# Kernel tuning notes

Hardware: AMD Instinct MI355X
Metric: run time of the kernel (lower is better)

## Reference

```python
import jax, jax.numpy as jnp
import numpy as np

B, C1, C2, H, W = 3, 256, 256, 48, 48
CC = 128      # c = int(c2*e)
NB = 2        # n blocks
HEADS = 4     # max(1, 128//32)
HD = CC // HEADS
SCALE = HD ** -0.5
EPS = 1e-5


def setup_inputs():
    key = jax.random.key(0)
    ks = iter(jax.random.split(key, 64))
    def rn(shape, scale=1.0):
        return jax.random.normal(next(ks), shape, jnp.float32) * scale
    s1 = 1.0 / np.sqrt(C1)
    sc = 1.0 / np.sqrt(CC)
    s2c = 1.0 / np.sqrt(2 * CC)
    s4c = 1.0 / np.sqrt(4 * CC)
    inp = {
        'x': rn((B, C1, H, W)),
        'cv1_w': rn((2 * CC, C1), s1),
        'cv1_g': 1.0 + rn((2 * CC,), 0.1), 'cv1_b': rn((2 * CC,), 0.1),
        'cv1_m': rn((2 * CC,), 0.1), 'cv1_v': 1.0 + 0.5 * jax.random.uniform(next(ks), (2 * CC,)),
        'n1_g': 1.0 + rn((NB, CC), 0.1), 'n1_b': rn((NB, CC), 0.1),
        'qkv_w': rn((NB, 3 * CC, CC), sc), 'qkv_b': rn((NB, 3 * CC), 0.02),
        'proj_w': rn((NB, CC, CC), sc), 'proj_b': rn((NB, CC), 0.02),
        'n2_g': 1.0 + rn((NB, CC), 0.1), 'n2_b': rn((NB, CC), 0.1),
        'f1_w': rn((NB, 2 * CC, CC), sc), 'f1_b': rn((NB, 2 * CC), 0.02),
        'f2_w': rn((NB, CC, 2 * CC), s2c), 'f2_b': rn((NB, CC), 0.02),
        'cv2_w': rn((C2, 4 * CC), s4c),
        'cv2_g': 1.0 + rn((C2,), 0.1), 'cv2_b': rn((C2,), 0.1),
        'cv2_m': rn((C2,), 0.1), 'cv2_v': 1.0 + 0.5 * jax.random.uniform(next(ks), (C2,)),
    }
    return inp


def conv1x1(x, w, b=None):
    y = jnp.einsum('bchw,oc->bohw', x, w)
    if b is not None:
        y = y + b[:, None, None]
    return y


def conv_bn_silu(x, w, g, b, m, v):
    y = conv1x1(x, w)
    y = (y - m[:, None, None]) / jnp.sqrt(v + EPS)[:, None, None] * g[:, None, None] + b[:, None, None]
    return jax.nn.silu(y)


def groupnorm1(x, g, b):
    mu = x.mean(axis=(1, 2, 3), keepdims=True)
    var = x.var(axis=(1, 2, 3), keepdims=True)
    return (x - mu) / jnp.sqrt(var + EPS) * g[:, None, None] + b[:, None, None]


def attention(x, qw, qb, pw, pb):
    # Faithful to torch code incl. the unbind(0)-over-batch quirk (requires B==3).
    b, c, h, w = x.shape
    qkv = conv1x1(x, qw, qb)                                   # (3, 3C, H, W)
    qkv = qkv.reshape(b, 3, HEADS, HD, h * w)                  # (B=3, 3, heads, hd, HW)
    q, k, v = qkv[0], qkv[1], qkv[2]                           # each (3, heads, hd, HW)
    attn = jnp.einsum('ghdn,ghdm->ghnm', q, k) * SCALE         # q.T @ k -> (3, heads, HW, HW)
    attn = jax.nn.softmax(attn, axis=-1)
    out = jnp.einsum('ghdm,ghnm->ghdn', v, attn)               # v @ attn.T -> (3, heads, hd, HW)
    out = out.transpose(0, 2, 1, 3).reshape(b, c, h, w)        # transpose(1,2).reshape
    return conv1x1(out, pw, pb)


def forward(x, cv1_w, cv1_g, cv1_b, cv1_m, cv1_v, n1_g, n1_b, qkv_w, qkv_b,
            proj_w, proj_b, n2_g, n2_b, f1_w, f1_b, f2_w, f2_b,
            cv2_w, cv2_g, cv2_b, cv2_m, cv2_v):
    y = conv_bn_silu(x, cv1_w, cv1_g, cv1_b, cv1_m, cv1_v)     # (B, 2c, H, W)
    y1, y2 = y[:, :CC], y[:, CC:]
    outs = [y1, y2]
    cur = y2
    for i in range(NB):
        a = attention(groupnorm1(cur, n1_g[i], n1_b[i]), qkv_w[i], qkv_b[i], proj_w[i], proj_b[i])
        cur = cur + a
        h2 = groupnorm1(cur, n2_g[i], n2_b[i])
        f = jax.nn.gelu(conv1x1(h2, f1_w[i], f1_b[i]), approximate=False)
        cur = cur + conv1x1(f, f2_w[i], f2_b[i])
        outs.append(cur)
    cat = jnp.concatenate(outs, axis=1)                        # (B, 4c, H, W)
    return conv_bn_silu(cat, cv2_w, cv2_g, cv2_b, cv2_m, cv2_v)


def reference(x, cv1_w, cv1_g, cv1_b, cv1_m, cv1_v, n1_g, n1_b, qkv_w, qkv_b,
              proj_w, proj_b, n2_g, n2_b, f1_w, f1_b, f2_w, f2_b,
              cv2_w, cv2_g, cv2_b, cv2_m, cv2_v):
    return forward(x, cv1_w, cv1_g, cv1_b, cv1_m, cv1_v, n1_g, n1_b, qkv_w, qkv_b,
                   proj_w, proj_b, n2_g, n2_b, f1_w, f1_b, f2_w, f2_b,
                   cv2_w, cv2_g, cv2_b, cv2_m, cv2_v)
```

## Files before the change

kernel.cpp:

```cpp
#include <hip/hip_runtime.h>
#include <hip/hip_bf16.h>
#include <math.h>

#define HW 2304
#define EPSV 1e-5f
#define INV_N (1.f / 294912.f)
#define QS_LOG2E (0.17677669529663687f * 1.44269504088896340f)
#define NSPLIT 4

enum { E_CV1 = 0, E_QKV = 1, E_RES = 2, E_F1 = 3, E_CV2 = 4 };

typedef __attribute__((ext_vector_type(8))) short bf16x8;
typedef __attribute__((ext_vector_type(4))) float f32x4;

static __device__ __forceinline__ ushort b16(float f) {
    union { __hip_bfloat16 h; ushort u; } cv;
    cv.h = __float2bfloat16(f);
    return cv.u;
}
static __device__ __forceinline__ float bf(ushort u) {
    union { unsigned u; float f; } c; c.u = (unsigned)u << 16; return c.f;
}
static __device__ __forceinline__ void stat_acc(float* STAT, int slot, int b,
                                                float s, float sq) {
    #pragma unroll
    for (int off = 32; off; off >>= 1) { s += __shfl_xor(s, off); sq += __shfl_xor(sq, off); }
    if ((threadIdx.x & 63) == 0) {
        atomicAdd(&STAT[(slot * 3 + b) * 2], s);
        atomicAdd(&STAT[(slot * 3 + b) * 2 + 1], sq);
    }
}

__global__ __launch_bounds__(256) void prep(
    const float* __restrict__ cv1w, const float* __restrict__ projw,
    const float* __restrict__ f2w, const float* __restrict__ cv2w,
    const float* __restrict__ qw, const float* __restrict__ g1, const float* __restrict__ b1,
    const float* __restrict__ fw1, const float* __restrict__ g2, const float* __restrict__ b2,
    const float* __restrict__ X,
    ushort* __restrict__ WB, ushort* __restrict__ FW, float* __restrict__ CV,
    ushort* __restrict__ XT, float* __restrict__ STAT)
{
    __shared__ ushort tb[64][68];
    const int bid = blockIdx.x, t = threadIdx.x;
    if (bid < 288) {
        if (bid == 0 && t < 32) STAT[t] = 0.f;
        const int idx = (bid * 256 + t) * 4;
        const float* src;
        int off;
        if      (idx < 65536)  { src = cv1w; off = 0; }
        else if (idx < 98304)  { src = projw; off = 65536; }
        else if (idx < 163840) { src = f2w;  off = 98304; }
        else                   { src = cv2w; off = 163840; }
        float4 v = *(const float4*)&src[idx - off];
        ushort4 u;
        u.x = b16(v.x); u.y = b16(v.y); u.z = b16(v.z); u.w = b16(v.w);
        *(ushort4*)&WB[idx] = u;
    } else if (bid < 608) {
        const int r = (bid - 288) * 4 + (t >> 6);
        const int lane = t & 63;
        const int i = r / 640, rr = r % 640;
        const float* wrow; const float* ga; const float* bb; ushort* dst;
        int cvs, cvb;
        if (rr < 384) {
            wrow = qw + ((size_t)i * 384 + rr) * 128;
            ga = g1 + i * 128; bb = b1 + i * 128;
            dst = FW + (size_t)i * 49152 + rr * 128;
            cvs = i * 1280 + rr; cvb = i * 1280 + 384 + rr;
        } else {
            const int o = rr - 384;
            wrow = fw1 + ((size_t)i * 256 + o) * 128;
            ga = g2 + i * 128; bb = b2 + i * 128;
            dst = FW + 98304 + (size_t)i * 32768 + o * 128;
            cvs = i * 1280 + 768 + o; cvb = i * 1280 + 1024 + o;
        }
        const float w0 = wrow[lane], w1 = wrow[lane + 64];
        const float p0 = w0 * ga[lane], p1 = w1 * ga[lane + 64];
        dst[lane] = b16(p0); dst[lane + 64] = b16(p1);
        float sw = p0 + p1;
        float wb = w0 * bb[lane] + w1 * bb[lane + 64];
        #pragma unroll
        for (int off = 32; off; off >>= 1) { sw += __shfl_xor(sw, off); wb += __shfl_xor(wb, off); }
        if (lane == 0) { CV[cvs] = sw; CV[cvb] = wb; }
    } else {
        const int flat = bid - 608;
        const int bx = flat % 36, by = (flat / 36) % 4, bz = flat / 144;
        const int cb = by * 64, nb = bx * 64;
        #pragma unroll
        for (int k = 0; k < 4; k++) {
            const int row = k * 16 + (t >> 4), cq = t & 15;
            float4 v = *(const float4*)&X[(size_t)(bz * 256 + cb + row) * HW + nb + cq * 4];
            ushort4 u; u.x = b16(v.x); u.y = b16(v.y); u.z = b16(v.z); u.w = b16(v.w);
            *(ushort4*)&tb[row][cq * 4] = u;
        }
        __syncthreads();
        #pragma unroll
        for (int k = 0; k < 4; k++) {
            const int n = k * 16 + (t >> 4), cq = t & 15;
            ushort4 u;
            u.x = tb[cq * 4 + 0][n]; u.y = tb[cq * 4 + 1][n];
            u.z = tb[cq * 4 + 2][n]; u.w = tb[cq * 4 + 3][n];
            *(ushort4*)&XT[((size_t)bz * HW + nb + n) * 256 + cb + cq * 4] = u;
        }
    }
}

template <int EPI>
__global__ __launch_bounds__(256) void gemm_mfma(
    const ushort* __restrict__ W, const ushort* __restrict__ X,
    int K, int xld, int xoff,
    const float* __restrict__ q0, const float* __restrict__ q1,
    const float* __restrict__ q2, const float* __restrict__ q3,
    float* __restrict__ STAT, int slotUse, int slotAcc,
    const float* __restrict__ cvec,
    ushort* __restrict__ CT, int rcol, int ycol,
    float* __restrict__ Yf,
    ushort* __restrict__ U0, ushort* __restrict__ U1, ushort* __restrict__ U2)
{
    const int b = blockIdx.z;
    const int t = threadIdx.x;
    const int w = t >> 6, l = t & 63;
    const int ln = l & 15, lg = l >> 4;
    const int wo = (w & 1) * 64, wn = (w >> 1) * 64;
    const int ob = blockIdx.y * 128 + wo;
    const int nb = blockIdx.x * 128 + wn;

    const ushort* ap = W + (size_t)(ob + ln) * K + lg * 8;
    const ushort* bp = X + ((size_t)b * HW + nb + ln) * xld + xoff + lg * 8;

    bf16x8 a0[4], bb0[4], a1[4], bb1[4];
    #pragma unroll
    for (int i = 0; i < 4; i++) {
        a0[i]  = *(const bf16x8*)(ap + (size_t)i * 16 * K);
        bb0[i] = *(const bf16x8*)(bp + (size_t)i * 16 * xld);
    }
    f32x4 acc[4][4];
    #pragma unroll
    for (int i = 0; i < 4; i++)
        #pragma unroll
        for (int j = 0; j < 4; j++) acc[i][j] = (f32x4){0.f, 0.f, 0.f, 0.f};

    for (int c0 = 32; c0 <= K; c0 += 32) {
        if (c0 < K) {
            #pragma unroll
            for (int i = 0; i < 4; i++) {
                a1[i]  = *(const bf16x8*)(ap + (size_t)i * 16 * K + c0);
                bb1[i] = *(const bf16x8*)(bp + (size_t)i * 16 * xld + c0);
            }
        }
        #pragma unroll
        for (int i = 0; i < 4; i++)
            #pragma unroll
            for (int j = 0; j < 4; j++)
                acc[i][j] = __builtin_amdgcn_mfma_f32_16x16x32_bf16(a0[i], bb0[j], acc[i][j], 0, 0, 0);
        #pragma unroll
        for (int i = 0; i < 4; i++) { a0[i] = a1[i]; bb0[i] = bb1[i]; }
    }

    float mu = 0.f, rs = 0.f;
    if (EPI == E_QKV || EPI == E_F1) {
        const float s  = STAT[(slotUse * 3 + b) * 2];
        const float sq = STAT[(slotUse * 3 + b) * 2 + 1];
        mu = s * INV_N;
        rs = rsqrtf(sq * INV_N - mu * mu + EPSV);
    }
    float ls = 0.f, lsq = 0.f;

    #pragma unroll
    for (int i = 0; i < 4; i++) {
        const int obase = ob + i * 16 + lg * 4;
        if (EPI == E_CV1 || EPI == E_CV2) {
            float sc[4], sh[4];
            #pragma unroll
            for (int r = 0; r < 4; r++) {
                const int o = obase + r;
                const float irs = rsqrtf(q3[o] + EPSV);
                sc[r] = q0[o] * irs;
                sh[r] = q1[o] - q2[o] * sc[r];
            }
            #pragma unroll
            for (int j = 0; j < 4; j++) {
                const int n = nb + j * 16 + ln;
                ushort4 u;
                #pragma unroll
                for (int r = 0; r < 4; r++) {
                    float y = fmaf(acc[i][j][r], sc[r], sh[r]);
                    y = y / (1.f + __expf(-y));
                    if (EPI == E_CV2) {
                        Yf[(size_t)(b * 256 + obase + r) * HW + n] = y;
                    } else {
                        ls += y; lsq += y * y;
                        if (r == 0) u.x = b16(y); else if (r == 1) u.y = b16(y);
                        else if (r == 2) u.z = b16(y); else u.w = b16(y);
                    }
                }
                if (EPI == E_CV1)
                    *(ushort4*)&CT[((size_t)b * HW + n) * 512 + ycol + obase] = u;
            }
        } else if (EPI == E_QKV) {
            const int gh = obase >> 5;
            const int d0 = obase & 31;
            float C[4];
            #pragma unroll
            for (int r = 0; r < 4; r++) {
                const int o = obase + r;
                C[r] = q0[o] + cvec[384 + o] - rs * mu * cvec[o];
            }
            #pragma unroll
            for (int j = 0; j < 4; j++) {
                const int n = nb + j * 16 + ln;
                float y0 = fmaf(rs, acc[i][j][0], C[0]);
                float y1 = fmaf(rs, acc[i][j][1], C[1]);
                float y2 = fmaf(rs, acc[i][j][2], C[2]);
                float y3 = fmaf(rs, acc[i][j][3], C[3]);
                if (b == 0) {
                    ushort4 u;
                    u.x = b16(y0 * QS_LOG2E); u.y = b16(y1 * QS_LOG2E);
                    u.z = b16(y2 * QS_LOG2E); u.w = b16(y3 * QS_LOG2E);
                    *(ushort4*)&U0[((size_t)gh * HW + n) * 32 + d0] = u;
                } else if (b == 1) {
                    ushort4 u;
                    u.x = b16(y0); u.y = b16(y1); u.z = b16(y2); u.w = b16(y3);
                    *(ushort4*)&U1[((size_t)gh * HW + n) * 32 + d0] = u;
                } else {
                    U2[(size_t)(obase + 0) * HW + n] = b16(y0);
                    U2[(size_t)(obase + 1) * HW + n] = b16(y1);
                    U2[(size_t)(obase + 2) * HW + n] = b16(y2);
                    U2[(size_t)(obase + 3) * HW + n] = b16(y3);
                }
            }
        } else if (EPI == E_RES) {
            #pragma unroll
            for (int j = 0; j < 4; j++) {
                const int n = nb + j * 16 + ln;
                const size_t base = ((size_t)b * HW + n) * 512;
                ushort4 rv = *(const ushort4*)&CT[base + rcol + obase];
                float y0 = acc[i][j][0] + q0[obase + 0] + bf(rv.x);
                float y1 = acc[i][j][1] + q0[obase + 1] + bf(rv.y);
                float y2 = acc[i][j][2] + q0[obase + 2] + bf(rv.z);
                float y3 = acc[i][j][3] + q0[obase + 3] + bf(rv.w);
                ls += (y0 + y1) + (y2 + y3);
                lsq += y0 * y0 + y1 * y1 + y2 * y2 + y3 * y3;
                ushort4 u;
                u.x = b16(y0); u.y = b16(y1); u.z = b16(y2); u.w = b16(y3);
                *(ushort4*)&CT[base + ycol + obase] = u;
            }
        } else {
            float C[4];
            #pragma unroll
            for (int r = 0; r < 4; r++) {
                const int o = obase + r;
                C[r] = q0[o] + cvec[256 + o] - rs * mu * cvec[o];
            }
            #pragma unroll
            for (int j = 0; j < 4; j++) {
                const int n = nb + j * 16 + ln;
                ushort4 u;
                #pragma unroll
                for (int r = 0; r < 4; r++) {
                    float y = fmaf(rs, acc[i][j][r], C[r]);
                    y = 0.5f * y * (1.f + erff(y * 0.70710678f));
                    if (r == 0) u.x = b16(y); else if (r == 1) u.y = b16(y);
                    else if (r == 2) u.z = b16(y); else u.w = b16(y);
                }
                *(ushort4*)&U0[((size_t)b * HW + n) * 256 + obase] = u;
            }
        }
    }
    if (EPI == E_CV1 && slotAcc >= 0 && blockIdx.y == 1) stat_acc(STAT, slotAcc, b, ls, lsq);
    if (EPI == E_RES && slotAcc >= 0) stat_acc(STAT, slotAcc, b, ls, lsq);
}

__global__ __launch_bounds__(256) void attn_mfma(
    const ushort* __restrict__ QT,
    const ushort* __restrict__ KT,
    const ushort* __restrict__ VB,
    float* __restrict__ POa,
    float* __restrict__ POb,
    float* __restrict__ MS)
{
    __shared__ __align__(16) ushort Kl[2][2048];
    __shared__ __align__(16) ushort Vl[2][2048];
    __shared__ __align__(16) ushort plds[4][16][72];
    const int gh = blockIdx.y, g = gh >> 2, h = gh & 3;
    const int sp = blockIdx.z;
    const int t = threadIdx.x, w = t >> 6, l = t & 63;
    const int ln = l & 15, lg = l >> 4;
    const int n0 = (blockIdx.x * 4 + w) * 16;
    const int ms0 = sp * 576, mend = ms0 + 576;

    const ushort* ktg = KT + (size_t)gh * HW * 32;
    const ushort* vg  = VB + ((size_t)g * 128 + h * 32) * HW;

    const int krow = t >> 2, kcq = t & 3;
    const int vrow = t >> 3, vcq = t & 7;
    const int kw = krow * 32 + ((kcq ^ (krow & 3)) << 3);
    const int vw = vrow * 64 + ((vcq ^ (vrow & 7)) << 3);
    const int krd = ln * 32 + ((lg ^ (ln & 3)) << 3);
    const int vs  = ln & 7;
    const int vrd0 = ln * 64 + ((lg ^ vs) << 3);
    const int vrd1 = ln * 64 + (((lg + 4) ^ vs) << 3);
    const int vrd2 = (16 + ln) * 64 + ((lg ^ vs) << 3);
    const int vrd3 = (16 + ln) * 64 + (((lg + 4) ^ vs) << 3);

    const bf16x8 qf = *(const bf16x8*)(QT + ((size_t)gh * HW + n0 + ln) * 32 + lg * 8);

    f32x4 o0 = {0.f, 0.f, 0.f, 0.f}, o1 = {0.f, 0.f, 0.f, 0.f};
    float M = -3.0e38f, S = 0.f;

    {
        bf16x8 kr = *(const bf16x8*)(ktg + (size_t)(ms0 + krow) * 32 + kcq * 8);
        bf16x8 vr = *(const bf16x8*)(vg + (size_t)vrow * HW + ms0 + vcq * 8);
        *(bf16x8*)&Kl[0][kw] = kr;
        *(bf16x8*)&Vl[0][vw] = vr;
    }
    int cur = 0;

    for (int m0 = ms0; m0 < mend; m0 += 64) {
        __syncthreads();
        const bool more = (m0 + 64 < mend);
        bf16x8 kr, vr;
        if (more) {
            kr = *(const bf16x8*)(ktg + (size_t)(m0 + 64 + krow) * 32 + kcq * 8);
            vr = *(const bf16x8*)(vg + (size_t)vrow * HW + m0 + 64 + vcq * 8);
        }

        f32x4 st[4];
        const f32x4 zero = {0.f, 0.f, 0.f, 0.f};
        #pragma unroll
        for (int mc = 0; mc < 4; mc++) {
            const bf16x8 kf = *(const bf16x8*)&Kl[cur][mc * 512 + krd];
            st[mc] = __builtin_amdgcn_mfma_f32_16x16x32_bf16(kf, qf, zero, 0, 0, 0);
        }

        float mx = st[0][0];
        #pragma unroll
        for (int mc = 0; mc < 4; mc++)
            #pragma unroll
            for (int r = 0; r < 4; r++) mx = fmaxf(mx, st[mc][r]);
        mx = fmaxf(mx, __shfl_xor(mx, 16));
        mx = fmaxf(mx, __shfl_xor(mx, 32));
        if (!__all(mx <= M + 8.f)) {
            const float Mn = fmaxf(M, mx);
            const float corr = exp2f(M - Mn);
            S *= corr;
            #pragma unroll
            for (int r = 0; r < 4; r++) { o0[r] *= corr; o1[r] *= corr; }
            M = Mn;
        }
        float ps = 0.f;
        ushort4 pw[4];
        #pragma unroll
        for (int mc = 0; mc < 4; mc++) {
            float p0v = exp2f(st[mc][0] - M), p1v = exp2f(st[mc][1] - M);
            float p2v = exp2f(st[mc][2] - M), p3v = exp2f(st[mc][3] - M);
            ps += (p0v + p1v) + (p2v + p3v);
            pw[mc].x = b16(p0v); pw[mc].y = b16(p1v);
            pw[mc].z = b16(p2v); pw[mc].w = b16(p3v);
        }
        ps += __shfl_xor(ps, 16);
        ps += __shfl_xor(ps, 32);
        S += ps;

        #pragma unroll
        for (int mc = 0; mc < 4; mc++)
            *(ushort4*)&plds[w][ln][mc * 16 + lg * 4] = pw[mc];
        bf16x8 pf0 = *(const bf16x8*)&plds[w][ln][lg * 8];
        bf16x8 pf1 = *(const bf16x8*)&plds[w][ln][32 + lg * 8];

        const bf16x8 vf0 = *(const bf16x8*)&Vl[cur][vrd0];
        const bf16x8 vf1 = *(const bf16x8*)&Vl[cur][vrd1];
        const bf16x8 vf2 = *(const bf16x8*)&Vl[cur][vrd2];
        const bf16x8 vf3 = *(const bf16x8*)&Vl[cur][vrd3];
        o0 = __builtin_amdgcn_mfma_f32_16x16x32_bf16(vf0, pf0, o0, 0, 0, 0);
        o0 = __builtin_amdgcn_mfma_f32_16x16x32_bf16(vf1, pf1, o0, 0, 0, 0);
        o1 = __builtin_amdgcn_mfma_f32_16x16x32_bf16(vf2, pf0, o1, 0, 0, 0);
        o1 = __builtin_amdgcn_mfma_f32_16x16x32_bf16(vf3, pf1, o1, 0, 0, 0);

        if (more) {
            *(bf16x8*)&Kl[cur ^ 1][kw] = kr;
            *(bf16x8*)&Vl[cur ^ 1][vw] = vr;
        }
        cur ^= 1;
    }

    float* po = (sp < 2) ? (POa + (size_t)sp * 884736)
                         : (POb + (size_t)(sp - 2) * 884736);
    #pragma unroll
    for (int r = 0; r < 4; r++) {
        const int d = lg * 4 + r;
        po[((size_t)gh * 32 + d) * HW + n0 + ln]      = o0[r];
        po[((size_t)gh * 32 + d + 16) * HW + n0 + ln] = o1[r];
    }
    if (lg == 0) {
        float* ms = MS + (((size_t)sp * 12 + gh) * HW + n0 + ln) * 2;
        ms[0] = M; ms[1] = S;
    }
}

__global__ __launch_bounds__(256) void merge_proj(
    const float* __restrict__ POa, const float* __restrict__ POb,
    const float* __restrict__ MS,
    const ushort* __restrict__ PW, const float* __restrict__ pb,
    ushort* __restrict__ CT, int rcol, int ycol,
    float* __restrict__ STAT, int slotAcc)
{
    __shared__ float fw[4][NSPLIT][64];
    __shared__ __align__(16) unsigned long long obuf[64][34];
    const int g = blockIdx.y, nb = blockIdx.x * 64;
    const int t = threadIdx.x;
    {
        const int h = t >> 6, nl = t & 63, gh = g * 4 + h, n = nb + nl;
        float Mk[NSPLIT], Sk[NSPLIT];
        #pragma unroll
        for (int k = 0; k < NSPLIT; k++) {
            Mk[k] = MS[(((size_t)k * 12 + gh) * HW + n) * 2 + 0];
            Sk[k] = MS[(((size_t)k * 12 + gh) * HW + n) * 2 + 1];
        }
        float Mx = Mk[0];
        #pragma unroll
        for (int k = 1; k < NSPLIT; k++) Mx = fmaxf(Mx, Mk[k]);
        float wk[NSPLIT], den = 0.f;
        #pragma unroll
        for (int k = 0; k < NSPLIT; k++) { wk[k] = exp2f(Mk[k] - Mx); den += Sk[k] * wk[k]; }
        const float inv = 1.f / den;
        #pragma unroll
        for (int k = 0; k < NSPLIT; k++) fw[h][k][nl] = wk[k] * inv;
    }
    __syncthreads();
    {
        const int nl = t & 63, dd = t >> 6;
        #pragma unroll
        for (int p = 0; p < 8; p++) {
            const int d = p * 4 + dd;
            ushort uu[4];
            #pragma unroll
            for (int h = 0; h < 4; h++) {
                const int gh = g * 4 + h;
                const size_t idx = ((size_t)gh * 32 + d) * HW + nb + nl;
                float v = 0.f;
                #pragma unroll
                for (int k = 0; k < 2; k++)
                    v += POa[(size_t)k * 884736 + idx] * fw[h][k][nl];
                #pragma unroll
                for (int k = 0; k < 2; k++)
                    v += POb[(size_t)k * 884736 + idx] * fw[h][k + 2][nl];
                uu[h] = b16(v);
            }
            obuf[nl][d] = (unsigned long long)uu[0] | ((unsigned long long)uu[1] << 16)
                        | ((unsigned long long)uu[2] << 32) | ((unsigned long long)uu[3] << 48);
        }
    }
    __syncthreads();
    const int w = t >> 6, l = t & 63, ln = l & 15, lg = l >> 4;
    const int wo = (w & 1) * 64, wn = (w >> 1) * 32;
    const ushort* ob_base = (const ushort*)&obuf[0][0];
    const ushort* ap = PW + (size_t)(wo + ln) * 128 + lg * 8;
    f32x4 acc[4][2];
    #pragma unroll
    for (int i = 0; i < 4; i++)
        #pragma unroll
        for (int jf = 0; jf < 2; jf++) acc[i][jf] = (f32x4){0.f, 0.f, 0.f, 0.f};
    #pragma unroll
    for (int kk = 0; kk < 4; kk++) {
        bf16x8 bfr[2];
        #pragma unroll
        for (int jf = 0; jf < 2; jf++)
            bfr[jf] = *(const bf16x8*)(ob_base + (wn + jf * 16 + ln) * 136 + kk * 32 + lg * 8);
        #pragma unroll
        for (int i = 0; i < 4; i++) {
            const bf16x8 af = *(const bf16x8*)(ap + (size_t)i * 16 * 128 + kk * 32);
            acc[i][0] = __builtin_amdgcn_mfma_f32_16x16x32_bf16(af, bfr[0], acc[i][0], 0, 0, 0);
            acc[i][1] = __builtin_amdgcn_mfma_f32_16x16x32_bf16(af, bfr[1], acc[i][1], 0, 0, 0);
        }
    }
    float ls = 0.f, lsq = 0.f;
    #pragma unroll
    for (int i = 0; i < 4; i++) {
        const int o4 = wo + i * 16 + lg * 4;
        #pragma unroll
        for (int jf = 0; jf < 2; jf++) {
            const int n = nb + wn + jf * 16 + ln;
            const size_t base = ((size_t)g * HW + n) * 512;
            ushort4 rv = *(const ushort4*)&CT[base + rcol + o4];
            float y0 = acc[i][jf][0] + pb[o4 + 0] + bf(rv.x);
            float y1 = acc[i][jf][1] + pb[o4 + 1] + bf(rv.y);
            float y2 = acc[i][jf][2] + pb[o4 + 2] + bf(rv.z);
            float y3 = acc[i][jf][3] + pb[o4 + 3] + bf(rv.w);
            ls += (y0 + y1) + (y2 + y3);
            lsq += y0 * y0 + y1 * y1 + y2 * y2 + y3 * y3;
            ushort4 u;
            u.x = b16(y0); u.y = b16(y1); u.z = b16(y2); u.w = b16(y3);
            *(ushort4*)&CT[base + ycol + o4] = u;
        }
    }
    stat_acc(STAT, slotAcc, g, ls, lsq);
}

extern "C" void kernel_launch(void* const* d_in, const int* in_sizes, int n_in,
                              void* d_out, int out_size, void* d_ws, size_t ws_size,
                              hipStream_t stream)
{
    (void)in_sizes; (void)n_in; (void)out_size; (void)ws_size;
    const float* x      = (const float*)d_in[0];
    const float* cv1_w  = (const float*)d_in[1];
    const float* cv1_g  = (const float*)d_in[2];
    const float* cv1_b  = (const float*)d_in[3];
    const float* cv1_m  = (const float*)d_in[4];
    const float* cv1_v  = (const float*)d_in[5];
    const float* n1_g   = (const float*)d_in[6];
    const float* n1_b   = (const float*)d_in[7];
    const float* qkv_w  = (const float*)d_in[8];
    const float* qkv_b  = (const float*)d_in[9];
    const float* proj_w = (const float*)d_in[10];
    const float* proj_b = (const float*)d_in[11];
    const float* n2_g   = (const float*)d_in[12];
    const float* n2_b   = (const float*)d_in[13];
    const float* f1_w   = (const float*)d_in[14];
    const float* f1_b   = (const float*)d_in[15];
    const float* f2_w   = (const float*)d_in[16];
    const float* f2_b   = (const float*)d_in[17];
    const float* cv2_w  = (const float*)d_in[18];
    const float* cv2_g  = (const float*)d_in[19];
    const float* cv2_b  = (const float*)d_in[20];
    const float* cv2_m  = (const float*)d_in[21];
    const float* cv2_v  = (const float*)d_in[22];
    float* out = (float*)d_out;

    float* ws = (float*)d_ws;
    ushort* CATT = (ushort*)ws;
    ushort* QT   = (ushort*)(ws + 1769472);
    ushort* KTb  = (ushort*)(ws + 2211840);
    ushort* VB   = (ushort*)(ws + 2654208);
    float*  MS   = ws + 3096576;
    ushort* WB   = (ushort*)(ws + 3428352);
    ushort* FW   = (ushort*)(ws + 3575808);
    float*  CV   = ws + 3657728;
    float*  STAT = ws + 3660288;
    float*  POb  = ws + 3660352;
    ushort* FT   = QT;
    ushort* XTX  = (ushort*)POb;
    float*  POa  = (float*)d_out;

    dim3 blk(256);

    prep<<<dim3(1040), blk, 0, stream>>>(
        cv1_w, proj_w, f2_w, cv2_w, qkv_w, n1_g, n1_b, f1_w, n2_g, n2_b,
        x, WB, FW, CV, XTX, STAT);

    gemm_mfma<E_CV1><<<dim3(18, 2, 3), blk, 0, stream>>>(
        WB + 0, XTX, 256, 256, 0, cv1_g, cv1_b, cv1_m, cv1_v,
        STAT, -1, 0, nullptr, CATT, 0, 0, nullptr, nullptr, nullptr, nullptr);

    for (int i = 0; i < 2; i++) {
        const int prev = (i == 0) ? 128 : 256;
        const int next = 256 + 128 * i;
        const int gn1 = (i == 0) ? 0 : 2;
        const int gn2 = (i == 0) ? 1 : 3;

        gemm_mfma<E_QKV><<<dim3(18, 3, 3), blk, 0, stream>>>(
            FW + (size_t)i * 49152, CATT, 128, 512, prev, qkv_b + i * 384,
            nullptr, nullptr, nullptr, STAT, gn1, -1, CV + i * 1280,
            nullptr, 0, 0, nullptr, QT, KTb, VB);
        attn_mfma<<<dim3(36, 12, NSPLIT), blk, 0, stream>>>(QT, KTb, VB, POa, POb, MS);
        merge_proj<<<dim3(36, 3), blk, 0, stream>>>(
            POa, POb, MS, WB + 65536 + (size_t)i * 16384, proj_b + i * 128,
            CATT, prev, next, STAT, gn2);

        gemm_mfma<E_F1><<<dim3(18, 2, 3), blk, 0, stream>>>(
            FW + 98304 + (size_t)i * 32768, CATT, 128, 512, next, f1_b + i * 256,
            nullptr, nullptr, nullptr, STAT, gn2, -1, CV + i * 1280 + 768,
            nullptr, 0, 0, nullptr, FT, nullptr, nullptr);
        gemm_mfma<E_RES><<<dim3(18, 1, 3), blk, 0, stream>>>(
            WB + 98304 + (size_t)i * 32768, FT, 256, 256, 0, f2_b + i * 128,
            nullptr, nullptr, nullptr, STAT, -1, (i == 0) ? 2 : -1, nullptr,
            CATT, next, next, nullptr, nullptr, nullptr, nullptr);
    }

    gemm_mfma<E_CV2><<<dim3(18, 2, 3), blk, 0, stream>>>(
        WB + 163840, CATT, 512, 512, 0, cv2_g, cv2_b, cv2_m, cv2_v,
        STAT, -1, -1, nullptr, nullptr, 0, 0, out, nullptr, nullptr, nullptr);
}
```

Baseline: 226.4 us.

## Fuse FFN f1/GELU/f2 GEMMs and final cv2 into one kernel per block

Replaces the separate F1 GEMM, F2 residual GEMM and final CV2 GEMM launches with a single ffn_fused kernel per block. Each 32-column tile computes the f1 output into LDS, runs f2 from LDS with the residual add, and in the last block also computes cv2 using the freshly written y tile from LDS. This removes the FT intermediate round trip through global memory and two to three kernel launches. In exchange the tiles are smaller (32 columns, 216 blocks), which lowers weight reuse and reloads the f1, f2 and cv2 weights from global memory for every tile.

```diff
diff --git a/kernel.cpp b/kernel.cpp
--- a/kernel.cpp
+++ b/kernel.cpp
@@ -8,7 +8,7 @@
 #define QS_LOG2E (0.17677669529663687f * 1.44269504088896340f)
 #define NSPLIT 4
 
-enum { E_CV1 = 0, E_QKV = 1, E_RES = 2, E_F1 = 3, E_CV2 = 4 };
+enum { E_CV1 = 0, E_QKV = 1 };
 
 typedef __attribute__((ext_vector_type(8))) short bf16x8;
 typedef __attribute__((ext_vector_type(4))) float f32x4;
@@ -112,8 +112,7 @@
     const float* __restrict__ q2, const float* __restrict__ q3,
     float* __restrict__ STAT, int slotUse, int slotAcc,
     const float* __restrict__ cvec,
-    ushort* __restrict__ CT, int rcol, int ycol,
-    float* __restrict__ Yf,
+    ushort* __restrict__ CT, int ycol,
     ushort* __restrict__ U0, ushort* __restrict__ U1, ushort* __restrict__ U2)
 {
     const int b = blockIdx.z;
@@ -157,7 +156,7 @@
     }
 
     float mu = 0.f, rs = 0.f;
-    if (EPI == E_QKV || EPI == E_F1) {
+    if (EPI == E_QKV) {
         const float s  = STAT[(slotUse * 3 + b) * 2];
         const float sq = STAT[(slotUse * 3 + b) * 2 + 1];
         mu = s * INV_N;
@@ -168,7 +167,7 @@
     #pragma unroll
     for (int i = 0; i < 4; i++) {
         const int obase = ob + i * 16 + lg * 4;
-        if (EPI == E_CV1 || EPI == E_CV2) {
+        if (EPI == E_CV1) {
             float sc[4], sh[4];
             #pragma unroll
             for (int r = 0; r < 4; r++) {
@@ -185,18 +184,13 @@
                 for (int r = 0; r < 4; r++) {
                     float y = fmaf(acc[i][j][r], sc[r], sh[r]);
                     y = y / (1.f + __expf(-y));
-                    if (EPI == E_CV2) {
-                        Yf[(size_t)(b * 256 + obase + r) * HW + n] = y;
-                    } else {
-                        ls += y; lsq += y * y;
-                        if (r == 0) u.x = b16(y); else if (r == 1) u.y = b16(y);
-                        else if (r == 2) u.z = b16(y); else u.w = b16(y);
-                    }
+                    ls += y; lsq += y * y;
+                    if (r == 0) u.x = b16(y); else if (r == 1) u.y = b16(y);
+                    else if (r == 2) u.z = b16(y); else u.w = b16(y);
                 }
-                if (EPI == E_CV1)
-                    *(ushort4*)&CT[((size_t)b * HW + n) * 512 + ycol + obase] = u;
-            }
-        } else if (EPI == E_QKV) {
+                *(ushort4*)&CT[((size_t)b * HW + n) * 512 + ycol + obase] = u;
+            }
+        } else {
             const int gh = obase >> 5;
             const int d0 = obase & 31;
             float C[4];
@@ -228,32 +222,67 @@
                     U2[(size_t)(obase + 3) * HW + n] = b16(y3);
                 }
             }
-        } else if (EPI == E_RES) {
-            #pragma unroll
-            for (int j = 0; j < 4; j++) {
-                const int n = nb + j * 16 + ln;
-                const size_t base = ((size_t)b * HW + n) * 512;
-                ushort4 rv = *(const ushort4*)&CT[base + rcol + obase];
-                float y0 = acc[i][j][0] + q0[obase + 0] + bf(rv.x);
-                float y1 = acc[i][j][1] + q0[obase + 1] + bf(rv.y);
-                float y2 = acc[i][j][2] + q0[obase + 2] + bf(rv.z);
-                float y3 = acc[i][j][3] + q0[obase + 3] + bf(rv.w);
-                ls += (y0 + y1) + (y2 + y3);
-                lsq += y0 * y0 + y1 * y1 + y2 * y2 + y3 * y3;
-                ushort4 u;
-                u.x = b16(y0); u.y = b16(y1); u.z = b16(y2); u.w = b16(y3);
-                *(ushort4*)&CT[base + ycol + obase] = u;
-            }
-        } else {
+        }
+    }
+    if (EPI == E_CV1 && slotAcc >= 0 && blockIdx.y == 1) stat_acc(STAT, slotAcc, b, ls, lsq);
+}
+
+template <int LAST>
+__global__ __launch_bounds__(256) void ffn_fused(
+    const ushort* __restrict__ FW1, const float* __restrict__ f1b,
+    const float* __restrict__ cvec,
+    const ushort* __restrict__ W2, const float* __restrict__ f2b,
+    ushort* __restrict__ CT, int col,
+    float* __restrict__ STAT, int slotUse, int slotAcc,
+    const ushort* __restrict__ WCV2, const float* __restrict__ q0,
+    const float* __restrict__ q1, const float* __restrict__ q2,
+    const float* __restrict__ q3, float* __restrict__ out)
+{
+    __shared__ __align__(16) ushort Fl[32][264];
+    __shared__ __align__(16) ushort Yl[32][136];
+    const int b = blockIdx.z, nb = blockIdx.x * 32;
+    const int t = threadIdx.x, w = t >> 6, l = t & 63;
+    const int ln = l & 15, lg = l >> 4;
+
+    const float s  = STAT[(slotUse * 3 + b) * 2];
+    const float sq = STAT[(slotUse * 3 + b) * 2 + 1];
+    const float mu = s * INV_N;
+    const float rs = rsqrtf(sq * INV_N - mu * mu + EPSV);
+
+    {
+        const int ob = w * 64;
+        const ushort* ap = FW1 + (size_t)(ob + ln) * 128 + lg * 8;
+        const ushort* bp = CT + ((size_t)b * HW + nb + ln) * 512 + col + lg * 8;
+        f32x4 acc[4][2];
+        #pragma unroll
+        for (int i = 0; i < 4; i++)
+            #pragma unroll
+            for (int j = 0; j < 2; j++) acc[i][j] = (f32x4){0.f, 0.f, 0.f, 0.f};
+        #pragma unroll
+        for (int kk = 0; kk < 4; kk++) {
+            bf16x8 bfr[2];
+            #pragma unroll
+            for (int j = 0; j < 2; j++)
+                bfr[j] = *(const bf16x8*)(bp + (size_t)(j * 16) * 512 + kk * 32);
+            #pragma unroll
+            for (int i = 0; i < 4; i++) {
+                const bf16x8 af = *(const bf16x8*)(ap + (size_t)(i * 16) * 128 + kk * 32);
+                acc[i][0] = __builtin_amdgcn_mfma_f32_16x16x32_bf16(af, bfr[0], acc[i][0], 0, 0, 0);
+                acc[i][1] = __builtin_amdgcn_mfma_f32_16x16x32_bf16(af, bfr[1], acc[i][1], 0, 0, 0);
+            }
+        }
+        #pragma unroll
+        for (int i = 0; i < 4; i++) {
+            const int obase = ob + i * 16 + lg * 4;
             float C[4];
             #pragma unroll
             for (int r = 0; r < 4; r++) {
                 const int o = obase + r;
-                C[r] = q0[o] + cvec[256 + o] - rs * mu * cvec[o];
-            }
-            #pragma unroll
-            for (int j = 0; j < 4; j++) {
-                const int n = nb + j * 16 + ln;
+                C[r] = f1b[o] + cvec[256 + o] - rs * mu * cvec[o];
+            }
+            #pragma unroll
+            for (int j = 0; j < 2; j++) {
+                const int n = j * 16 + ln;
                 ushort4 u;
                 #pragma unroll
                 for (int r = 0; r < 4; r++) {
@@ -262,12 +291,127 @@
                     if (r == 0) u.x = b16(y); else if (r == 1) u.y = b16(y);
                     else if (r == 2) u.z = b16(y); else u.w = b16(y);
                 }
-                *(ushort4*)&U0[((size_t)b * HW + n) * 256 + obase] = u;
-            }
-        }
-    }
-    if (EPI == E_CV1 && slotAcc >= 0 && blockIdx.y == 1) stat_acc(STAT, slotAcc, b, ls, lsq);
-    if (EPI == E_RES && slotAcc >= 0) stat_acc(STAT, slotAcc, b, ls, lsq);
+                *(ushort4*)&Fl[n][obase] = u;
+            }
+        }
+    }
+    __syncthreads();
+
+    float ls = 0.f, lsq = 0.f;
+    {
+        const int wo = w * 32;
+        const ushort* ap = W2 + (size_t)(wo + ln) * 256 + lg * 8;
+        f32x4 acc[2][2];
+        #pragma unroll
+        for (int i = 0; i < 2; i++)
+            #pragma unroll
+            for (int j = 0; j < 2; j++) acc[i][j] = (f32x4){0.f, 0.f, 0.f, 0.f};
+        #pragma unroll
+        for (int kk = 0; kk < 8; kk++) {
+            bf16x8 bfr[2];
+            #pragma unroll
+            for (int j = 0; j < 2; j++)
+                bfr[j] = *(const bf16x8*)&Fl[j * 16 + ln][kk * 32 + lg * 8];
+            #pragma unroll
+            for (int i = 0; i < 2; i++) {
+                const bf16x8 af = *(const bf16x8*)(ap + (size_t)(i * 16) * 256 + kk * 32);
+                acc[i][0] = __builtin_amdgcn_mfma_f32_16x16x32_bf16(af, bfr[0], acc[i][0], 0, 0, 0);
+                acc[i][1] = __builtin_amdgcn_mfma_f32_16x16x32_bf16(af, bfr[1], acc[i][1], 0, 0, 0);
+            }
+        }
+        #pragma unroll
+        for (int i = 0; i < 2; i++) {
+            const int o4 = wo + i * 16 + lg * 4;
+            #pragma unroll
+            for (int j = 0; j < 2; j++) {
+                const int n = nb + j * 16 + ln;
+                ushort* cp = &CT[((size_t)b * HW + n) * 512 + col + o4];
+                ushort4 rv = *(const ushort4*)cp;
+                float y0 = acc[i][j][0] + f2b[o4 + 0] + bf(rv.x);
+                float y1 = acc[i][j][1] + f2b[o4 + 1] + bf(rv.y);
+                float y2 = acc[i][j][2] + f2b[o4 + 2] + bf(rv.z);
+                float y3 = acc[i][j][3] + f2b[o4 + 3] + bf(rv.w);
+                ls += (y0 + y1) + (y2 + y3);
+                lsq += y0 * y0 + y1 * y1 + y2 * y2 + y3 * y3;
+                ushort4 u;
+                u.x = b16(y0); u.y = b16(y1); u.z = b16(y2); u.w = b16(y3);
+                *(ushort4*)cp = u;
+                if (LAST) *(ushort4*)&Yl[j * 16 + ln][o4] = u;
+            }
+        }
+    }
+    if (slotAcc >= 0) stat_acc(STAT, slotAcc, b, ls, lsq);
+
+    if (LAST) {
+        __syncthreads();
+        const int ob = w * 64;
+        const ushort* ap = WCV2 + (size_t)(ob + ln) * 512 + lg * 8;
+        const ushort* bp = CT + ((size_t)b * HW + nb + ln) * 512 + lg * 8;
+        f32x4 acc[4][2];
+        #pragma unroll
+        for (int i = 0; i < 4; i++)
+            #pragma unroll
+            for (int j = 0; j < 2; j++) acc[i][j] = (f32x4){0.f, 0.f, 0.f, 0.f};
+        bf16x8 a0[4], b0[2], a1[4], b1[2];
+        #pragma unroll
+        for (int i = 0; i < 4; i++) a0[i] = *(const bf16x8*)(ap + (size_t)(i * 16) * 512);
+        #pragma unroll
+        for (int j = 0; j < 2; j++) b0[j] = *(const bf16x8*)(bp + (size_t)(j * 16) * 512);
+        for (int c0 = 32; c0 <= 384; c0 += 32) {
+            if (c0 < 384) {
+                #pragma unroll
+                for (int i = 0; i < 4; i++)
+                    a1[i] = *(const bf16x8*)(ap + (size_t)(i * 16) * 512 + c0);
+                #pragma unroll
+                for (int j = 0; j < 2; j++)
+                    b1[j] = *(const bf16x8*)(bp + (size_t)(j * 16) * 512 + c0);
+            }
+            #pragma unroll
+            for (int i = 0; i < 4; i++) {
+                acc[i][0] = __builtin_amdgcn_mfma_f32_16x16x32_bf16(a0[i], b0[0], acc[i][0], 0, 0, 0);
+                acc[i][1] = __builtin_amdgcn_mfma_f32_16x16x32_bf16(a0[i], b0[1], acc[i][1], 0, 0, 0);
+            }
+            #pragma unroll
+            for (int i = 0; i < 4; i++) a0[i] = a1[i];
+            #pragma unroll
+            for (int j = 0; j < 2; j++) b0[j] = b1[j];
+        }
+        #pragma unroll
+        for (int kk = 0; kk < 4; kk++) {
+            bf16x8 bfr[2];
+            #pragma unroll
+            for (int j = 0; j < 2; j++)
+                bfr[j] = *(const bf16x8*)&Yl[j * 16 + ln][kk * 32 + lg * 8];
+            #pragma unroll
+            for (int i = 0; i < 4; i++) {
+                const bf16x8 af = *(const bf16x8*)(ap + (size_t)(i * 16) * 512 + 384 + kk * 32);
+                acc[i][0] = __builtin_amdgcn_mfma_f32_16x16x32_bf16(af, bfr[0], acc[i][0], 0, 0, 0);
+                acc[i][1] = __builtin_amdgcn_mfma_f32_16x16x32_bf16(af, bfr[1], acc[i][1], 0, 0, 0);
+            }
+        }
+        #pragma unroll
+        for (int i = 0; i < 4; i++) {
+            const int obase = ob + i * 16 + lg * 4;
+            float sc[4], sh[4];
+            #pragma unroll
+            for (int r = 0; r < 4; r++) {
+                const int o = obase + r;
+                const float irs = rsqrtf(q3[o] + EPSV);
+                sc[r] = q0[o] * irs;
+                sh[r] = q1[o] - q2[o] * sc[r];
+            }
+            #pragma unroll
+            for (int j = 0; j < 2; j++) {
+                const int n = nb + j * 16 + ln;
+                #pragma unroll
+                for (int r = 0; r < 4; r++) {
+                    float y = fmaf(acc[i][j][r], sc[r], sh[r]);
+                    y = y / (1.f + __expf(-y));
+                    out[(size_t)(b * 256 + obase + r) * HW + n] = y;
+                }
+            }
+        }
+    }
 }
 
 __global__ __launch_bounds__(256) void attn_mfma(
@@ -537,7 +681,6 @@
     float*  CV   = ws + 3657728;
     float*  STAT = ws + 3660288;
     float*  POb  = ws + 3660352;
-    ushort* FT   = QT;
     ushort* XTX  = (ushort*)POb;
     float*  POa  = (float*)d_out;
 
@@ -549,7 +692,7 @@
 
     gemm_mfma<E_CV1><<<dim3(18, 2, 3), blk, 0, stream>>>(
         WB + 0, XTX, 256, 256, 0, cv1_g, cv1_b, cv1_m, cv1_v,
-        STAT, -1, 0, nullptr, CATT, 0, 0, nullptr, nullptr, nullptr, nullptr);
+        STAT, -1, 0, nullptr, CATT, 0, nullptr, nullptr, nullptr);
 
     for (int i = 0; i < 2; i++) {
         const int prev = (i == 0) ? 128 : 256;
@@ -560,23 +703,22 @@
         gemm_mfma<E_QKV><<<dim3(18, 3, 3), blk, 0, stream>>>(
             FW + (size_t)i * 49152, CATT, 128, 512, prev, qkv_b + i * 384,
             nullptr, nullptr, nullptr, STAT, gn1, -1, CV + i * 1280,
-            nullptr, 0, 0, nullptr, QT, KTb, VB);
+            nullptr, 0, QT, KTb, VB);
         attn_mfma<<<dim3(36, 12, NSPLIT), blk, 0, stream>>>(QT, KTb, VB, POa, POb, MS);
         merge_proj<<<dim3(36, 3), blk, 0, stream>>>(
             POa, POb, MS, WB + 65536 + (size_t)i * 16384, proj_b + i * 128,
             CATT, prev, next, STAT, gn2);
 
-        gemm_mfma<E_F1><<<dim3(18, 2, 3), blk, 0, stream>>>(
-            FW + 98304 + (size_t)i * 32768, CATT, 128, 512, next, f1_b + i * 256,
-            nullptr, nullptr, nullptr, STAT, gn2, -1, CV + i * 1280 + 768,
-            nullptr, 0, 0, nullptr, FT, nullptr, nullptr);
-        gemm_mfma<E_RES><<<dim3(18, 1, 3), blk, 0, stream>>>(
-            WB + 98304 + (size_t)i * 32768, FT, 256, 256, 0, f2_b + i * 128,
-            nullptr, nullptr, nullptr, STAT, -1, (i == 0) ? 2 : -1, nullptr,
-            CATT, next, next, nullptr, nullptr, nullptr, nullptr);
-    }
-
-    gemm_mfma<E_CV2><<<dim3(18, 2, 3), blk, 0, stream>>>(
-        WB + 163840, CATT, 512, 512, 0, cv2_g, cv2_b, cv2_m, cv2_v,
-        STAT, -1, -1, nullptr, nullptr, 0, 0, out, nullptr, nullptr, nullptr);
-}
+        if (i == 0) {
+            ffn_fused<0><<<dim3(72, 1, 3), blk, 0, stream>>>(
+                FW + 98304, f1_b, CV + 768,
+                WB + 98304, f2_b, CATT, 256, STAT, 1, 2,
+                nullptr, nullptr, nullptr, nullptr, nullptr, nullptr);
+        } else {
+            ffn_fused<1><<<dim3(72, 1, 3), blk, 0, stream>>>(
+                FW + 98304 + 32768, f1_b + 256, CV + 1280 + 768,
+                WB + 98304 + 32768, f2_b + 128, CATT, 384, STAT, 3, -1,
+                WB + 163840, cv2_g, cv2_b, cv2_m, cv2_v, out);
+        }
+    }
+}
```

Result: faster. 198.6 us (-12.3%).
